# Kernel optimization log

Hardware: AMD Instinct MI355X
Metric: run time of the kernel (lower is better)

Reference implementation:

```python
import jax, jax.numpy as jnp
import numpy as np

N_NODES = 50000
D = 64            # encoder.out_node_dim
N_EDGES = 800000
HID = 64          # mlp_edge_model_dim


def setup_inputs() -> dict:
    key = jax.random.key(0)
    k1, k2, k3, k4 = jax.random.split(key, 4)
    node_emb = jax.random.normal(k1, (N_NODES, D), dtype=jnp.float32)
    edge_index = jax.random.randint(k2, (2, N_EDGES), 0, N_NODES, dtype=jnp.int64)
    # Xavier-uniform style init for the 2-layer edge MLP
    lim1 = np.sqrt(6.0 / (2 * D + HID)).astype(np.float32)
    lim2 = np.sqrt(6.0 / (HID + 1)).astype(np.float32)
    W1 = jax.random.uniform(k3, (2 * D, HID), minval=-lim1, maxval=lim1, dtype=jnp.float32)
    b1 = jnp.zeros((HID,), dtype=jnp.float32)
    W2 = jax.random.uniform(k4, (HID, 1), minval=-lim2, maxval=lim2, dtype=jnp.float32)
    b2 = jnp.zeros((1,), dtype=jnp.float32)
    return {"node_emb": node_emb, "edge_index": edge_index,
            "W1": W1, "b1": b1, "W2": W2, "b2": b2}


def reference(node_emb, edge_index, W1, b1, W2, b2):
    src, dst = edge_index[0], edge_index[1]
    emb_src = node_emb[src]              # [E, D] gather
    emb_dst = node_emb[dst]              # [E, D] gather
    edge_emb = jnp.concatenate([emb_src, emb_dst], axis=1)  # [E, 2D]
    h = jax.nn.relu(edge_emb @ W1 + b1)  # [E, HID]
    edge_logits = h @ W2 + b2            # [E, 1]
    return edge_logits
```

## Files before the change

kernel.cpp:

```cpp
#include <hip/hip_runtime.h>


typedef __attribute__((ext_vector_type(8))) short short8;
typedef __attribute__((ext_vector_type(4))) float f32x4;
typedef __attribute__((ext_vector_type(8))) _Float16 half8;

__device__ __forceinline__ unsigned short f2bf_rne(float f) {
    union { float f; unsigned u; } v;
    v.f = f;
    return (unsigned short)((v.u + 0x7FFFu + ((v.u >> 16) & 1u)) >> 16);
}

#define W1T_K 72
#define CT_STRIDE 136

__global__ __launch_bounds__(256)
void node_uv(const float* __restrict__ X,
             const float* __restrict__ W1,
             const float* __restrict__ b1,
             _Float16* __restrict__ UV,
             int nnodes, int ntiles) {
    __shared__ __align__(16) unsigned short w1t[128 * W1T_K];
    __shared__ __align__(16) _Float16 cbuf[4][16 * CT_STRIDE];

    const int tid = threadIdx.x;
#pragma unroll
    for (int i = 0; i < 32; ++i) {
        int idx = tid + i * 256;
        int r = idx >> 6;
        int col = idx & 63;
        int k = r & 63;
        int jp = col + (r & 64);
        w1t[jp * W1T_K + k] = f2bf_rne(W1[idx]);
    }
    __syncthreads();

    const int lane = tid & 63;
    const int wid = tid >> 6;
    const int c = lane & 15;
    const int quad = lane >> 4;

    const int t = blockIdx.x * 4 + wid;
    if (t >= ntiles) return;

    short8 bfrag[8][2];
#pragma unroll
    for (int nt = 0; nt < 8; ++nt)
#pragma unroll
        for (int kc = 0; kc < 2; ++kc)
            bfrag[nt][kc] =
                *(const short8*)&w1t[(nt * 16 + c) * W1T_K + kc * 32 + quad * 8];

    float b1v[8];
#pragma unroll
    for (int nt = 0; nt < 8; ++nt)
        b1v[nt] = (nt < 4) ? b1[nt * 16 + c] : 0.f;

    int n = t * 16 + c;
    n = (n < nnodes) ? n : (nnodes - 1);
    const float* xr = X + (size_t)n * 64 + quad * 8;
    f32x4 x0a = *(const f32x4*)(xr);
    f32x4 x0b = *(const f32x4*)(xr + 4);
    f32x4 x1a = *(const f32x4*)(xr + 32);
    f32x4 x1b = *(const f32x4*)(xr + 36);
    short8 a0, a1;
#pragma unroll
    for (int i = 0; i < 4; ++i) {
        a0[i] = (short)f2bf_rne(x0a[i]);
        a0[4 + i] = (short)f2bf_rne(x0b[i]);
        a1[i] = (short)f2bf_rne(x1a[i]);
        a1[4 + i] = (short)f2bf_rne(x1b[i]);
    }

    f32x4 acc[8];
#pragma unroll
    for (int nt = 0; nt < 8; ++nt) acc[nt] = (f32x4){0.f, 0.f, 0.f, 0.f};
#pragma unroll
    for (int nt = 0; nt < 8; ++nt) {
        acc[nt] = __builtin_amdgcn_mfma_f32_16x16x32_bf16(a0, bfrag[nt][0], acc[nt], 0, 0, 0);
        acc[nt] = __builtin_amdgcn_mfma_f32_16x16x32_bf16(a1, bfrag[nt][1], acc[nt], 0, 0, 0);
    }

    _Float16* cb = cbuf[wid];
#pragma unroll
    for (int nt = 0; nt < 8; ++nt)
#pragma unroll
        for (int r = 0; r < 4; ++r)
            cb[(quad * 4 + r) * CT_STRIDE + nt * 16 + c] =
                (_Float16)(acc[nt][r] + b1v[nt]);

    __builtin_amdgcn_s_waitcnt(0);

    const _Float16* rp = &cb[(lane >> 2) * CT_STRIDE + (lane & 3) * 32];
    const f32x4* s4 = (const f32x4*)rp;
    f32x4* dst = (f32x4*)(UV + (size_t)t * 2048 + lane * 32);
    dst[0] = s4[0];
    dst[1] = s4[1];
    dst[2] = s4[2];
    dst[3] = s4[3];
}

__global__ __launch_bounds__(256)
void edge_out(const int* __restrict__ eidx,
              const _Float16* __restrict__ UV,
              const float* __restrict__ W2,
              const float* __restrict__ b2,
              float* __restrict__ out, int E, int Ehalf) {
    int tid = blockIdx.x * 256 + threadIdx.x;
    int e0 = tid >> 3;
    int j = tid & 7;
    if (e0 >= Ehalf) return;
    int e1 = e0 + Ehalf;
    bool has1 = (e1 < E);

    int s0 = __builtin_nontemporal_load(eidx + e0);
    int d0 = __builtin_nontemporal_load(eidx + E + e0);
    int e1c = has1 ? e1 : e0;
    int s1 = __builtin_nontemporal_load(eidx + e1c);
    int d1 = __builtin_nontemporal_load(eidx + E + e1c);

    half8 u0 = *(const half8*)(UV + (size_t)s0 * 128 + j * 8);
    half8 v0 = *(const half8*)(UV + (size_t)d0 * 128 + 64 + j * 8);
    half8 u1 = *(const half8*)(UV + (size_t)s1 * 128 + j * 8);
    half8 v1 = *(const half8*)(UV + (size_t)d1 * 128 + 64 + j * 8);

    f32x4 w2a = *(const f32x4*)(W2 + j * 8);
    f32x4 w2b = *(const f32x4*)(W2 + j * 8 + 4);
    const float b2v = b2[0];

    float a0 = 0.f, a1 = 0.f;
#pragma unroll
    for (int i = 0; i < 4; ++i) {
        a0 = fmaf(fmaxf((float)u0[i] + (float)v0[i], 0.f), w2a[i], a0);
        a0 = fmaf(fmaxf((float)u0[4 + i] + (float)v0[4 + i], 0.f), w2b[i], a0);
        a1 = fmaf(fmaxf((float)u1[i] + (float)v1[i], 0.f), w2a[i], a1);
        a1 = fmaf(fmaxf((float)u1[4 + i] + (float)v1[4 + i], 0.f), w2b[i], a1);
    }
    a0 += __shfl_xor(a0, 1, 8);
    a0 += __shfl_xor(a0, 2, 8);
    a0 += __shfl_xor(a0, 4, 8);
    a1 += __shfl_xor(a1, 1, 8);
    a1 += __shfl_xor(a1, 2, 8);
    a1 += __shfl_xor(a1, 4, 8);
    if (j == 0) {
        __builtin_nontemporal_store(a0 + b2v, out + e0);
        if (has1) __builtin_nontemporal_store(a1 + b2v, out + e1);
    }
}

extern "C" void kernel_launch(void* const* d_in, const int* in_sizes, int n_in,
                              void* d_out, int out_size, void* d_ws, size_t ws_size,
                              hipStream_t stream) {
    const float* X = (const float*)d_in[0];
    const int* eidx = (const int*)d_in[1];
    const float* W1 = (const float*)d_in[2];
    const float* b1 = (const float*)d_in[3];
    const float* W2 = (const float*)d_in[4];
    const float* b2 = (const float*)d_in[5];
    float* out = (float*)d_out;

    const int nnodes = in_sizes[0] / 64;
    const int E = in_sizes[1] / 2;

    _Float16* UV = (_Float16*)d_ws;

    const int ntiles = (nnodes + 15) / 16;
    node_uv<<<(ntiles + 3) / 4, 256, 0, stream>>>(X, W1, b1, UV, nnodes, ntiles);

    const int Ehalf = (E + 1) / 2;
    const int nthreads = Ehalf * 8;
    edge_out<<<(nthreads + 255) / 256, 256, 0, stream>>>(eidx, UV, W2, b2, out, E, Ehalf);
}
```

Baseline: 103.0 us.

## Bin edges by (src,dst) node slice to localize UV gathers

Adds a binning pass that sorts edges into 64 buckets keyed by the source and destination node slices and writes (src,dst,edge) records. A second kernel then processes each bucket so that gathered UV rows come from a small node range, improving cache locality. Buckets that overflow their fixed capacity fall back to a slow scalar path inside the binning kernel. The cost is an extra kernel launch, atomics, and writing and reading about 12.8MB of records.

```diff
diff --git a/kernel.cpp b/kernel.cpp
--- a/kernel.cpp
+++ b/kernel.cpp
@@ -13,17 +13,29 @@
 
 #define W1T_K 72
 #define CT_STRIDE 136
+
+#define NBUCK 64
+#define CAP 16384
+#define CPB 256
+#define SLICE_M 687195u
+
+#define UV_OFF   0
+#define CUR_OFF  (16u * 1024 * 1024)
+#define REC_OFF  (CUR_OFF + 4096)
 
 __global__ __launch_bounds__(256)
 void node_uv(const float* __restrict__ X,
              const float* __restrict__ W1,
              const float* __restrict__ b1,
              _Float16* __restrict__ UV,
+             int* __restrict__ cur,
              int nnodes, int ntiles) {
     __shared__ __align__(16) unsigned short w1t[128 * W1T_K];
     __shared__ __align__(16) _Float16 cbuf[4][16 * CT_STRIDE];
 
     const int tid = threadIdx.x;
+    if (blockIdx.x == 0 && tid < NBUCK) cur[tid] = 0;
+
 #pragma unroll
     for (int i = 0; i < 32; ++i) {
         int idx = tid + i * 256;
@@ -101,32 +113,92 @@
 }
 
 __global__ __launch_bounds__(256)
-void edge_out(const int* __restrict__ eidx,
+void edge_bin(const int* __restrict__ eidx,
               const _Float16* __restrict__ UV,
               const float* __restrict__ W2,
               const float* __restrict__ b2,
-              float* __restrict__ out, int E, int Ehalf) {
-    int tid = blockIdx.x * 256 + threadIdx.x;
-    int e0 = tid >> 3;
-    int j = tid & 7;
-    if (e0 >= Ehalf) return;
-    int e1 = e0 + Ehalf;
-    bool has1 = (e1 < E);
-
-    int s0 = __builtin_nontemporal_load(eidx + e0);
-    int d0 = __builtin_nontemporal_load(eidx + E + e0);
-    int e1c = has1 ? e1 : e0;
-    int s1 = __builtin_nontemporal_load(eidx + e1c);
-    int d1 = __builtin_nontemporal_load(eidx + E + e1c);
-
-    half8 u0 = *(const half8*)(UV + (size_t)s0 * 128 + j * 8);
-    half8 v0 = *(const half8*)(UV + (size_t)d0 * 128 + 64 + j * 8);
-    half8 u1 = *(const half8*)(UV + (size_t)s1 * 128 + j * 8);
-    half8 v1 = *(const half8*)(UV + (size_t)d1 * 128 + 64 + j * 8);
-
-    f32x4 w2a = *(const f32x4*)(W2 + j * 8);
-    f32x4 w2b = *(const f32x4*)(W2 + j * 8 + 4);
+              int* __restrict__ cur,
+              int4* __restrict__ recs,
+              float* __restrict__ out, int E) {
+    __shared__ int lhist[NBUCK], lbase[NBUCK], loff[NBUCK];
+    const int tid = threadIdx.x;
+    if (tid < NBUCK) { lhist[tid] = 0; loff[tid] = 0; }
+    __syncthreads();
+
+    const int base = blockIdx.x * 1024;
+    int s[4], d[4], bk[4];
+#pragma unroll
+    for (int i = 0; i < 4; ++i) {
+        int e = base + i * 256 + tid;
+        if (e < E) {
+            s[i] = __builtin_nontemporal_load(eidx + e);
+            d[i] = __builtin_nontemporal_load(eidx + E + e);
+            bk[i] = (int)(__umulhi((unsigned)s[i], SLICE_M) * 8u +
+                          __umulhi((unsigned)d[i], SLICE_M));
+            atomicAdd(&lhist[bk[i]], 1);
+        } else {
+            bk[i] = -1;
+        }
+    }
+    __syncthreads();
+    if (tid < NBUCK && lhist[tid] > 0)
+        lbase[tid] = atomicAdd(&cur[tid], lhist[tid]);
+    __syncthreads();
+#pragma unroll
+    for (int i = 0; i < 4; ++i) {
+        if (bk[i] < 0) continue;
+        int e = base + i * 256 + tid;
+        int slot = lbase[bk[i]] + atomicAdd(&loff[bk[i]], 1);
+        if (slot < CAP) {
+            recs[bk[i] * CAP + slot] = make_int4(s[i], d[i], e, 0);
+        } else {
+            float acc = 0.f;
+            const _Float16* up = UV + (size_t)s[i] * 128;
+            const _Float16* vp = UV + (size_t)d[i] * 128 + 64;
+            for (int k = 0; k < 64; ++k)
+                acc += fmaxf((float)up[k] + (float)vp[k], 0.f) * W2[k];
+            out[e] = acc + b2[0];
+        }
+    }
+}
+
+__global__ __launch_bounds__(256)
+void edge_gather(const int4* __restrict__ recs,
+                 const int* __restrict__ cur,
+                 const _Float16* __restrict__ UV,
+                 const float* __restrict__ W2,
+                 const float* __restrict__ b2,
+                 float* __restrict__ out) {
+    const int tid = threadIdx.x;
+    const int sb = blockIdx.x & 7;
+    const int r = blockIdx.x >> 3;
+    const int db = r >> 8;
+    const int chunk = r & (CPB - 1);
+    const int b = sb * 8 + db;
+    const int cnt = min(cur[b], CAP);
+    const int w0 = chunk * 64;
+    if (w0 >= cnt) return;
+
+    const int slot = tid >> 3;
+    const int j = tid & 7;
+    const int4* rb = recs + (size_t)b * CAP;
+    const f32x4 w2a = *(const f32x4*)(W2 + j * 8);
+    const f32x4 w2b = *(const f32x4*)(W2 + j * 8 + 4);
     const float b2v = b2[0];
+
+    int ea = w0 + slot;
+    int eb = w0 + 32 + slot;
+    const bool va = ea < cnt;
+    const bool vb = eb < cnt;
+    ea = va ? ea : 0;
+    eb = vb ? eb : 0;
+    const int4 ra = rb[ea];
+    const int4 rc = rb[eb];
+
+    half8 u0 = *(const half8*)(UV + (size_t)ra.x * 128 + j * 8);
+    half8 v0 = *(const half8*)(UV + (size_t)ra.y * 128 + 64 + j * 8);
+    half8 u1 = *(const half8*)(UV + (size_t)rc.x * 128 + j * 8);
+    half8 v1 = *(const half8*)(UV + (size_t)rc.y * 128 + 64 + j * 8);
 
     float a0 = 0.f, a1 = 0.f;
 #pragma unroll
@@ -143,8 +215,8 @@
     a1 += __shfl_xor(a1, 2, 8);
     a1 += __shfl_xor(a1, 4, 8);
     if (j == 0) {
-        __builtin_nontemporal_store(a0 + b2v, out + e0);
-        if (has1) __builtin_nontemporal_store(a1 + b2v, out + e1);
+        if (va) out[ra.z] = a0 + b2v;
+        if (vb) out[rc.z] = a1 + b2v;
     }
 }
 
@@ -162,12 +234,16 @@
     const int nnodes = in_sizes[0] / 64;
     const int E = in_sizes[1] / 2;
 
-    _Float16* UV = (_Float16*)d_ws;
+    char* ws = (char*)d_ws;
+    _Float16* UV = (_Float16*)(ws + UV_OFF);
+    int* cur = (int*)(ws + CUR_OFF);
+    int4* recs = (int4*)(ws + REC_OFF);
 
     const int ntiles = (nnodes + 15) / 16;
-    node_uv<<<(ntiles + 3) / 4, 256, 0, stream>>>(X, W1, b1, UV, nnodes, ntiles);
-
-    const int Ehalf = (E + 1) / 2;
-    const int nthreads = Ehalf * 8;
-    edge_out<<<(nthreads + 255) / 256, 256, 0, stream>>>(eidx, UV, W2, b2, out, E, Ehalf);
-}
+    node_uv<<<(ntiles + 3) / 4, 256, 0, stream>>>(X, W1, b1, UV, cur, nnodes, ntiles);
+
+    const int nbin = (E + 1023) / 1024;
+    edge_bin<<<nbin, 256, 0, stream>>>(eidx, UV, W2, b2, cur, recs, out, E);
+
+    edge_gather<<<NBUCK * CPB, 256, 0, stream>>>(recs, cur, UV, W2, b2, out);
+}
```

Result: slower. 125.7 us (+22.1%).

## Convert edge kernel to grid-stride loop with software-pipelined index and gather loads

Applied to the files above, without the earlier changes.

The edge kernel now runs a capped grid of 2048 blocks with a grid-stride loop. It no longer gives each thread group a fixed pair of edges. Each iteration prefetches the next edge's embedding rows and the index pair two steps ahead, overlapping gather latency with the current edge's compute. This cuts block launch overhead and keeps loads in flight, but it also lowers total parallelism and serializes work per thread, which may reduce the memory-level parallelism that the previous two-edges-per-thread launch exposed.

```diff
diff --git a/kernel.cpp b/kernel.cpp
--- a/kernel.cpp
+++ b/kernel.cpp
@@ -105,46 +105,53 @@
               const _Float16* __restrict__ UV,
               const float* __restrict__ W2,
               const float* __restrict__ b2,
-              float* __restrict__ out, int E, int Ehalf) {
-    int tid = blockIdx.x * 256 + threadIdx.x;
+              float* __restrict__ out, int E) {
+    const int tid = blockIdx.x * 256 + threadIdx.x;
+    const int j = tid & 7;
+    const int step = (gridDim.x * 256) >> 3;
+
     int e0 = tid >> 3;
-    int j = tid & 7;
-    if (e0 >= Ehalf) return;
-    int e1 = e0 + Ehalf;
-    bool has1 = (e1 < E);
+    if (e0 >= E) return;
+
+    const f32x4 w2a = *(const f32x4*)(W2 + j * 8);
+    const f32x4 w2b = *(const f32x4*)(W2 + j * 8 + 4);
+    const float b2v = b2[0];
 
     int s0 = __builtin_nontemporal_load(eidx + e0);
     int d0 = __builtin_nontemporal_load(eidx + E + e0);
-    int e1c = has1 ? e1 : e0;
+    half8 u0 = *(const half8*)(UV + (size_t)s0 * 128 + j * 8);
+    half8 v0 = *(const half8*)(UV + (size_t)d0 * 128 + 64 + j * 8);
+
+    int e1 = e0 + step;
+    bool m1 = e1 < E;
+    int e1c = m1 ? e1 : e0;
     int s1 = __builtin_nontemporal_load(eidx + e1c);
     int d1 = __builtin_nontemporal_load(eidx + E + e1c);
 
-    half8 u0 = *(const half8*)(UV + (size_t)s0 * 128 + j * 8);
-    half8 v0 = *(const half8*)(UV + (size_t)d0 * 128 + 64 + j * 8);
-    half8 u1 = *(const half8*)(UV + (size_t)s1 * 128 + j * 8);
-    half8 v1 = *(const half8*)(UV + (size_t)d1 * 128 + 64 + j * 8);
+    while (true) {
+        half8 u1 = *(const half8*)(UV + (size_t)s1 * 128 + j * 8);
+        half8 v1 = *(const half8*)(UV + (size_t)d1 * 128 + 64 + j * 8);
 
-    f32x4 w2a = *(const f32x4*)(W2 + j * 8);
-    f32x4 w2b = *(const f32x4*)(W2 + j * 8 + 4);
-    const float b2v = b2[0];
+        int e2 = e1 + step;
+        bool m2 = m1 && (e2 < E);
+        int e2c = m2 ? e2 : e0;
+        int s2 = __builtin_nontemporal_load(eidx + e2c);
+        int d2 = __builtin_nontemporal_load(eidx + E + e2c);
 
-    float a0 = 0.f, a1 = 0.f;
+        float a = 0.f;
 #pragma unroll
-    for (int i = 0; i < 4; ++i) {
-        a0 = fmaf(fmaxf((float)u0[i] + (float)v0[i], 0.f), w2a[i], a0);
-        a0 = fmaf(fmaxf((float)u0[4 + i] + (float)v0[4 + i], 0.f), w2b[i], a0);
-        a1 = fmaf(fmaxf((float)u1[i] + (float)v1[i], 0.f), w2a[i], a1);
-        a1 = fmaf(fmaxf((float)u1[4 + i] + (float)v1[4 + i], 0.f), w2b[i], a1);
-    }
-    a0 += __shfl_xor(a0, 1, 8);
-    a0 += __shfl_xor(a0, 2, 8);
-    a0 += __shfl_xor(a0, 4, 8);
-    a1 += __shfl_xor(a1, 1, 8);
-    a1 += __shfl_xor(a1, 2, 8);
-    a1 += __shfl_xor(a1, 4, 8);
-    if (j == 0) {
-        __builtin_nontemporal_store(a0 + b2v, out + e0);
-        if (has1) __builtin_nontemporal_store(a1 + b2v, out + e1);
+        for (int i = 0; i < 4; ++i) {
+            a = fmaf(fmaxf((float)u0[i] + (float)v0[i], 0.f), w2a[i], a);
+            a = fmaf(fmaxf((float)u0[4 + i] + (float)v0[4 + i], 0.f), w2b[i], a);
+        }
+        a += __shfl_xor(a, 1, 8);
+        a += __shfl_xor(a, 2, 8);
+        a += __shfl_xor(a, 4, 8);
+        if (j == 0) __builtin_nontemporal_store(a + b2v, out + e0);
+
+        if (!m1) break;
+        e0 = e1; u0 = u1; v0 = v1;
+        e1 = e2; m1 = m2; s1 = s2; d1 = d2;
     }
 }
 
@@ -167,7 +174,8 @@
     const int ntiles = (nnodes + 15) / 16;
     node_uv<<<(ntiles + 3) / 4, 256, 0, stream>>>(X, W1, b1, UV, nnodes, ntiles);
 
-    const int Ehalf = (E + 1) / 2;
-    const int nthreads = Ehalf * 8;
-    edge_out<<<(nthreads + 255) / 256, 256, 0, stream>>>(eidx, UV, W2, b2, out, E, Ehalf);
+    int nthreads = E * 8;
+    int grid = (nthreads + 255) / 256;
+    if (grid > 2048) grid = 2048;
+    edge_out<<<grid, 256, 0, stream>>>(eidx, UV, W2, b2, out, E);
 }
```

Measured after the change: 105.2 us. 2.2% more time.
